# Kernel tuning notes

Hardware: AMD Instinct MI355X
Metric: run time of the kernel (lower is better)

## Reference

```python
import jax, jax.numpy as jnp
import numpy as np

NUM_HEADS = 16
HEAD_DIM = 64
EMBED_DIM = 1024
BSZ = 4
SEQ = 2048


def setup_inputs() -> dict:
    key = jax.random.key(0)
    ks = jax.random.split(key, 6)
    scale = 1.0 / np.sqrt(EMBED_DIM)
    return {
        "x": jax.random.normal(ks[0], (BSZ, SEQ, EMBED_DIM), jnp.float32),
        "rel_pos_bias": jax.random.normal(ks[1], (1, NUM_HEADS, SEQ, SEQ), jnp.float32),
        "Wq": jax.random.normal(ks[2], (EMBED_DIM, EMBED_DIM), jnp.float32) * scale,
        "Wk": jax.random.normal(ks[3], (EMBED_DIM, EMBED_DIM), jnp.float32) * scale,
        "Wv": jax.random.normal(ks[4], (EMBED_DIM, EMBED_DIM), jnp.float32) * scale,
        "Wo": jax.random.normal(ks[5], (EMBED_DIM, EMBED_DIM), jnp.float32) * scale,
    }


def reference(x, rel_pos_bias, Wq, Wk, Wv, Wo):
    b, s, e = x.shape
    h, d = NUM_HEADS, HEAD_DIM
    # projections (T5 linears have no bias); torch Linear: x @ W.T
    q = (x @ Wq.T).reshape(b, s, h, d).transpose(0, 2, 1, 3)  # [b,h,s,d]
    k = (x @ Wk.T).reshape(b, s, h, d).transpose(0, 2, 1, 3)
    v = (x @ Wv.T).reshape(b, s, h, d).transpose(0, 2, 1, 3)
    # unscaled attention scores + additive relative-position bias
    scores = jnp.einsum("bhqd,bhkd->bhqk", q, k) + rel_pos_bias  # [b,h,s,s]
    weights = jax.nn.softmax(scores.astype(jnp.float32), axis=-1).astype(scores.dtype)
    attn = jnp.einsum("bhqk,bhkd->bhqd", weights, v)  # [b,h,s,d]
    attn = attn.transpose(0, 2, 1, 3).reshape(b, s, e)
    return attn @ Wo.T
```

## Files before the change

kernel.cpp:

```cpp
#include <hip/hip_runtime.h>
#include <hip/hip_bf16.h>

#define NH 16
#define HD 64
#define ED 1024
#define BS 4
#define SL 2048

typedef _Float16 f16x8 __attribute__((ext_vector_type(8)));
typedef _Float16 f16x4 __attribute__((ext_vector_type(4)));
typedef _Float16 f16x2 __attribute__((ext_vector_type(2)));
typedef float floatx4 __attribute__((ext_vector_type(4)));

__global__ __launch_bounds__(256) void cvtw_kernel(const float* __restrict__ Wq,
                                                   const float* __restrict__ Wk,
                                                   const float* __restrict__ Wv,
                                                   _Float16* __restrict__ Wh)
{
    const float* W = (blockIdx.y == 0) ? Wq : (blockIdx.y == 1) ? Wk : Wv;
    _Float16* out = Wh + (size_t)blockIdx.y * (ED * ED);
    const int i = (blockIdx.x * 256 + threadIdx.x) * 4;
    float4 v = *(const float4*)(W + i);
    f16x4 c;
    c[0] = (_Float16)v.x; c[1] = (_Float16)v.y;
    c[2] = (_Float16)v.z; c[3] = (_Float16)v.w;
    *(f16x4*)(out + i) = c;
}

__device__ __forceinline__ int lds_boff(int kq, int rc)
{
    return (((kq << 7) + rc) << 4) ^ (kq << 5);
}

template <int A_MODE, int B_MODE, int OUT_MODE>
__device__ __forceinline__ void gemm128_body(const float* __restrict__ Af,
                                             const _Float16* __restrict__ Ah,
                                             const float* __restrict__ Bf,
                                             const _Float16* __restrict__ Bh,
                                             _Float16* __restrict__ outH,
                                             float* __restrict__ outF,
                                             int K, int N)
{
    __shared__ __align__(16) _Float16 As[4 * 128 * 8];
    __shared__ __align__(16) _Float16 Bs[4 * 128 * 8];

    const int tid  = threadIdx.x;
    const int wave = tid >> 6;
    const int lane = tid & 63;
    const int lo16 = lane & 15;
    const int hi4  = lane >> 4;
    const int wm = wave >> 1;
    const int wn = wave & 1;
    const int rowTile = blockIdx.y * 128;
    const int colTile = blockIdx.x * 128;

    floatx4 acc[4][4];
#pragma unroll
    for (int m = 0; m < 4; m++)
#pragma unroll
        for (int n = 0; n < 4; n++)
            acc[m][n] = (floatx4){0.f, 0.f, 0.f, 0.f};

    for (int kb = 0; kb < K; kb += 32) {
        float4 aF[4]; f16x8 aH[2];
        if (A_MODE == 0) {
#pragma unroll
            for (int r = 0; r < 4; r++) {
                const int t2 = tid + r * 256;
                const int row = t2 >> 3;
                const int k4 = (t2 & 7) * 4;
                aF[r] = *(const float4*)(Af + (size_t)(rowTile + row) * K + kb + k4);
            }
        } else {
#pragma unroll
            for (int r = 0; r < 2; r++) {
                const int t2 = tid + r * 256;
                const int row = t2 >> 2;
                const int ko = (t2 & 3) * 8;
                const int gr = rowTile + row;
                const int b = gr >> 11;
                const int s = gr & (SL - 1);
                const int k0 = kb + ko;
                const int h = k0 >> 6;
                const int d = k0 & (HD - 1);
                aH[r] = *(const f16x8*)(Ah + (((size_t)(b * NH + h)) * SL + s) * HD + d);
            }
        }
        f16x8 bH[2]; float4 bF[4];
        if (B_MODE == 0) {
#pragma unroll
            for (int r = 0; r < 2; r++) {
                const int t2 = tid + r * 256;
                const int col = t2 >> 2;
                const int ko = (t2 & 3) * 8;
                bH[r] = *(const f16x8*)(Bh + (size_t)(colTile + col) * K + kb + ko);
            }
        } else {
#pragma unroll
            for (int r = 0; r < 4; r++) {
                const int t2 = tid + r * 256;
                const int col = t2 >> 3;
                const int k4 = (t2 & 7) * 4;
                bF[r] = *(const float4*)(Bf + (size_t)(colTile + col) * K + kb + k4);
            }
        }

        __syncthreads();
        if (A_MODE == 0) {
#pragma unroll
            for (int r = 0; r < 4; r++) {
                const int t2 = tid + r * 256;
                const int row = t2 >> 3;
                const int k4 = (t2 & 7) * 4;
                f16x4 c;
                c[0] = (_Float16)aF[r].x; c[1] = (_Float16)aF[r].y;
                c[2] = (_Float16)aF[r].z; c[3] = (_Float16)aF[r].w;
                *(f16x4*)((char*)As + lds_boff(k4 >> 3, row) + (k4 & 7) * 2) = c;
            }
        } else {
#pragma unroll
            for (int r = 0; r < 2; r++) {
                const int t2 = tid + r * 256;
                const int row = t2 >> 2;
                const int ko = (t2 & 3) * 8;
                *(f16x8*)((char*)As + lds_boff(ko >> 3, row)) = aH[r];
            }
        }
        if (B_MODE == 0) {
#pragma unroll
            for (int r = 0; r < 2; r++) {
                const int t2 = tid + r * 256;
                const int col = t2 >> 2;
                const int ko = (t2 & 3) * 8;
                *(f16x8*)((char*)Bs + lds_boff(ko >> 3, col)) = bH[r];
            }
        } else {
#pragma unroll
            for (int r = 0; r < 4; r++) {
                const int t2 = tid + r * 256;
                const int col = t2 >> 3;
                const int k4 = (t2 & 7) * 4;
                f16x4 c;
                c[0] = (_Float16)bF[r].x; c[1] = (_Float16)bF[r].y;
                c[2] = (_Float16)bF[r].z; c[3] = (_Float16)bF[r].w;
                *(f16x4*)((char*)Bs + lds_boff(k4 >> 3, col) + (k4 & 7) * 2) = c;
            }
        }
        __syncthreads();

        f16x8 af[4], bfr[4];
#pragma unroll
        for (int m = 0; m < 4; m++)
            af[m] = *(const f16x8*)((char*)As + lds_boff(hi4, wm * 64 + m * 16 + lo16));
#pragma unroll
        for (int n = 0; n < 4; n++)
            bfr[n] = *(const f16x8*)((char*)Bs + lds_boff(hi4, wn * 64 + n * 16 + lo16));
#pragma unroll
        for (int m = 0; m < 4; m++)
#pragma unroll
            for (int n = 0; n < 4; n++)
                acc[m][n] = __builtin_amdgcn_mfma_f32_16x16x32_f16(af[m], bfr[n], acc[m][n], 0, 0, 0);
    }

#pragma unroll
    for (int m = 0; m < 4; m++) {
#pragma unroll
        for (int n = 0; n < 4; n++) {
            const int col = colTile + wn * 64 + n * 16 + lo16;
#pragma unroll
            for (int i = 0; i < 4; i++) {
                const int row = rowTile + wm * 64 + m * 16 + hi4 * 4 + i;
                float v = acc[m][n][i];
                if (OUT_MODE == 0) {
                    int b = row >> 11;
                    int s = row & (SL - 1);
                    int h = col >> 6;
                    int d = col & (HD - 1);
                    outH[(((size_t)(b * NH + h)) * SL + s) * HD + d] = (_Float16)v;
                } else {
                    outF[(size_t)row * N + col] = v;
                }
            }
        }
    }
}

__global__ __launch_bounds__(256) void qkv_kernel(const float* __restrict__ x,
                                                  const _Float16* __restrict__ Wh,
                                                  _Float16* __restrict__ Q,
                                                  _Float16* __restrict__ Kk,
                                                  _Float16* __restrict__ V)
{
    const _Float16* W = Wh + (size_t)blockIdx.z * (ED * ED);
    _Float16* out = (blockIdx.z == 0) ? Q : (blockIdx.z == 1) ? Kk : V;
    gemm128_body<0, 0, 0>(x, nullptr, nullptr, W, out, nullptr, ED, ED);
}

__global__ __launch_bounds__(256) void oproj_kernel(const _Float16* __restrict__ A,
                                                    const float* __restrict__ Wo,
                                                    float* __restrict__ out)
{
    gemm128_body<1, 1, 1>(nullptr, A, Wo, nullptr, nullptr, out, ED, ED);
}

__global__ __launch_bounds__(256) void attn_kernel(const _Float16* __restrict__ Qg,
                                                   const _Float16* __restrict__ Kg,
                                                   const _Float16* __restrict__ Vg,
                                                   const float* __restrict__ bias,
                                                   _Float16* __restrict__ attnOut)
{
    __shared__ __align__(16) _Float16 Ks[8 * 64 * 8];
    __shared__ __align__(16) _Float16 Vt[64 * 64];
    __shared__ __align__(16) _Float16 Ps[4 * 32 * 64];

    const int b  = blockIdx.x;
    const int qt = blockIdx.y;
    const int h  = blockIdx.z;
    const int bh = b * NH + h;
    const int tid  = threadIdx.x;
    const int wave = tid >> 6;
    const int lane = tid & 63;
    const int lo16 = lane & 15;
    const int hi4  = lane >> 4;

    const _Float16* Qbh = Qg + (size_t)bh * SL * HD;
    const _Float16* Kbh = Kg + (size_t)bh * SL * HD;
    const _Float16* Vbh = Vg + (size_t)bh * SL * HD;
    const float* biasH = bias + (size_t)h * SL * SL;

    const int q0 = qt * 128 + wave * 32;

    f16x8 qf[2][2];
#pragma unroll
    for (int m = 0; m < 2; m++)
#pragma unroll
        for (int ks = 0; ks < 2; ks++)
            qf[m][ks] = *(const f16x8*)(Qbh + (size_t)(q0 + m * 16 + lo16) * HD
                                        + ks * 32 + hi4 * 8);

    floatx4 oAcc[2][4];
    float mRow[2][4], lRow[2][4];
#pragma unroll
    for (int m = 0; m < 2; m++)
#pragma unroll
        for (int n = 0; n < 4; n++)
            oAcc[m][n] = (floatx4){0.f, 0.f, 0.f, 0.f};
#pragma unroll
    for (int m = 0; m < 2; m++)
#pragma unroll
        for (int r = 0; r < 4; r++) { mRow[m][r] = -1e30f; lRow[m][r] = 0.f; }

    const int kKey = tid >> 2;
    const int kD0  = (tid & 3) * 8;
    _Float16* kDst0 = Ks + (((kKey >> 4)     ) * 64 + (kKey & 15) + 16 * (kD0 >> 3)) * 8;
    _Float16* kDst1 = Ks + (((kKey >> 4) + 4) * 64 + (kKey & 15) + 16 * (kD0 >> 3)) * 8;

    const int vK0 = (tid >> 3) * 2;
    const int vD0 = (tid & 7) * 8;

    for (int kc = 0; kc < SL; kc += 64) {
        f16x8 ka = *(const f16x8*)(Kbh + (size_t)(kc + kKey) * HD + kD0);
        f16x8 kb = *(const f16x8*)(Kbh + (size_t)(kc + kKey) * HD + kD0 + 32);
        f16x8 va = *(const f16x8*)(Vbh + (size_t)(kc + vK0    ) * HD + vD0);
        f16x8 vb = *(const f16x8*)(Vbh + (size_t)(kc + vK0 + 1) * HD + vD0);

        __syncthreads();
        *(f16x8*)kDst0 = ka;
        *(f16x8*)kDst1 = kb;
#pragma unroll
        for (int i = 0; i < 8; i++) {
            const int d = vD0 + i;
            const int sw = (d & 7) ^ ((d >> 3) & 7);
            char* p = (char*)Vt + (d << 7)
                      + ((((vK0 >> 3) ^ sw) & 7) << 4) + ((vK0 & 7) << 1);
            f16x2 pr; pr[0] = va[i]; pr[1] = vb[i];
            *(f16x2*)p = pr;
        }
        __syncthreads();

        floatx4 s[2][4];
#pragma unroll
        for (int m = 0; m < 2; m++)
#pragma unroll
            for (int n = 0; n < 4; n++)
                s[m][n] = (floatx4){0.f, 0.f, 0.f, 0.f};
#pragma unroll
        for (int ks = 0; ks < 2; ks++)
#pragma unroll
            for (int n = 0; n < 4; n++) {
                f16x8 kf = *(const f16x8*)(Ks + ((ks * 4 + n) * 64 + lane) * 8);
                s[0][n] = __builtin_amdgcn_mfma_f32_16x16x32_f16(qf[0][ks], kf, s[0][n], 0, 0, 0);
                s[1][n] = __builtin_amdgcn_mfma_f32_16x16x32_f16(qf[1][ks], kf, s[1][n], 0, 0, 0);
            }

#pragma unroll
        for (int m = 0; m < 2; m++)
#pragma unroll
            for (int r = 0; r < 4; r++) {
                const int ql = m * 16 + hi4 * 4 + r;
                const float* bp = biasH + (size_t)(q0 + ql) * SL + kc + lo16;
                float s0 = s[m][0][r] + bp[0];
                float s1 = s[m][1][r] + bp[16];
                float s2 = s[m][2][r] + bp[32];
                float s3 = s[m][3][r] + bp[48];
                float rmax = fmaxf(fmaxf(s0, s1), fmaxf(s2, s3));
                rmax = fmaxf(rmax, __shfl_xor(rmax, 1));
                rmax = fmaxf(rmax, __shfl_xor(rmax, 2));
                rmax = fmaxf(rmax, __shfl_xor(rmax, 4));
                rmax = fmaxf(rmax, __shfl_xor(rmax, 8));
                const float mOld = mRow[m][r];
                const float mNew = fmaxf(mOld, rmax);
                const float alpha = __expf(mOld - mNew);
                mRow[m][r] = mNew;
                float p0 = __expf(s0 - mNew);
                float p1 = __expf(s1 - mNew);
                float p2 = __expf(s2 - mNew);
                float p3 = __expf(s3 - mNew);
                float rsum = (p0 + p1) + (p2 + p3);
                rsum += __shfl_xor(rsum, 1);
                rsum += __shfl_xor(rsum, 2);
                rsum += __shfl_xor(rsum, 4);
                rsum += __shfl_xor(rsum, 8);
                lRow[m][r] = lRow[m][r] * alpha + rsum;
#pragma unroll
                for (int n = 0; n < 4; n++) oAcc[m][n][r] *= alpha;

                char* pb = (char*)Ps + (wave << 12) + (ql << 7) + ((lo16 & 7) << 1);
                const int kb3 = lo16 >> 3;
                const int swp = (ql & 7) ^ (((ql >> 3) & 3) << 1);
                *(_Float16*)(pb + ((((0 + kb3) ^ swp) & 7) << 4)) = (_Float16)p0;
                *(_Float16*)(pb + ((((2 + kb3) ^ swp) & 7) << 4)) = (_Float16)p1;
                *(_Float16*)(pb + ((((4 + kb3) ^ swp) & 7) << 4)) = (_Float16)p2;
                *(_Float16*)(pb + ((((6 + kb3) ^ swp) & 7) << 4)) = (_Float16)p3;
            }

#pragma unroll
        for (int ks = 0; ks < 2; ks++) {
            f16x8 pa[2];
#pragma unroll
            for (int m = 0; m < 2; m++) {
                const int qlr = m * 16 + lo16;
                const int swp = (qlr & 7) ^ (((qlr >> 3) & 3) << 1);
                pa[m] = *(const f16x8*)((char*)Ps + (wave << 12) + (qlr << 7)
                                        + ((((ks * 4 + hi4) ^ swp) & 7) << 4));
            }
#pragma unroll
            for (int n = 0; n < 4; n++) {
                const int dv = n * 16 + lo16;
                const int swv = (dv & 7) ^ ((dv >> 3) & 7);
                f16x8 vf = *(const f16x8*)((char*)Vt + (dv << 7)
                                           + ((((ks * 4 + hi4) ^ swv) & 7) << 4));
                oAcc[0][n] = __builtin_amdgcn_mfma_f32_16x16x32_f16(pa[0], vf, oAcc[0][n], 0, 0, 0);
                oAcc[1][n] = __builtin_amdgcn_mfma_f32_16x16x32_f16(pa[1], vf, oAcc[1][n], 0, 0, 0);
            }
        }
    }

#pragma unroll
    for (int m = 0; m < 2; m++)
#pragma unroll
        for (int r = 0; r < 4; r++) {
            const float inv = 1.f / lRow[m][r];
            const int q = q0 + m * 16 + hi4 * 4 + r;
#pragma unroll
            for (int n = 0; n < 4; n++)
                attnOut[((size_t)bh * SL + q) * HD + n * 16 + lo16] =
                    (_Float16)(oAcc[m][n][r] * inv);
        }
}

extern "C" void kernel_launch(void* const* d_in, const int* in_sizes, int n_in,
                              void* d_out, int out_size, void* d_ws, size_t ws_size,
                              hipStream_t stream)
{
    (void)in_sizes; (void)n_in; (void)out_size; (void)ws_size;

    const float* x    = (const float*)d_in[0];
    const float* bias = (const float*)d_in[1];
    const float* Wq   = (const float*)d_in[2];
    const float* Wk   = (const float*)d_in[3];
    const float* Wv   = (const float*)d_in[4];
    const float* Wo   = (const float*)d_in[5];

    const size_t nQKV = (size_t)BS * NH * SL * HD;
    _Float16* Qh = (_Float16*)d_out;
    _Float16* Kh = Qh + nQKV;
    _Float16* Vh = (_Float16*)d_ws;
    _Float16* slotB = Vh + nQKV;
    _Float16* Wh = slotB;
    _Float16* attnH = slotB;

    cvtw_kernel<<<dim3(ED * ED / 1024, 3), 256, 0, stream>>>(Wq, Wk, Wv, Wh);

    dim3 gq(ED / 128, (BS * SL) / 128, 3);
    qkv_kernel<<<gq, 256, 0, stream>>>(x, Wh, Qh, Kh, Vh);

    dim3 ga(BS, SL / 128, NH);
    attn_kernel<<<ga, 256, 0, stream>>>(Qh, Kh, Vh, bias, attnH);

    dim3 go(ED / 128, (BS * SL) / 128);
    oproj_kernel<<<go, 256, 0, stream>>>(attnH, Wo, (float*)d_out);
}
```

Before: 747.6 us.

## Stage bias through LDS as fp16, prefetch K/V, lazy softmax rescale

The attention kernel now loads each 128x64 bias tile cooperatively with coalesced float4 reads, converts it to fp16 and stores it in a padded shared buffer instead of doing scattered per-lane global bias reads. K/V tiles for the next chunk are register-prefetched after the barrier so their loads overlap with compute. The online softmax skips the rescale unless the running max grows by more than 8, MFMA sections get raised wave priority, and the grid order is changed so q-tiles vary fastest. Rounding the bias to fp16 and deferring the rescale add numerical error, and the extra shared buffer may reduce occupancy.

```diff
diff --git a/kernel.cpp b/kernel.cpp
--- a/kernel.cpp
+++ b/kernel.cpp
@@ -212,9 +212,10 @@
     __shared__ __align__(16) _Float16 Ks[8 * 64 * 8];
     __shared__ __align__(16) _Float16 Vt[64 * 64];
     __shared__ __align__(16) _Float16 Ps[4 * 32 * 64];
-
-    const int b  = blockIdx.x;
-    const int qt = blockIdx.y;
+    __shared__ __align__(16) _Float16 Bi[128 * 68];
+
+    const int qt = blockIdx.x;
+    const int b  = blockIdx.y;
     const int h  = blockIdx.z;
     const int bh = b * NH + h;
     const int tid  = threadIdx.x;
@@ -254,15 +255,23 @@
     const int kD0  = (tid & 3) * 8;
     _Float16* kDst0 = Ks + (((kKey >> 4)     ) * 64 + (kKey & 15) + 16 * (kD0 >> 3)) * 8;
     _Float16* kDst1 = Ks + (((kKey >> 4) + 4) * 64 + (kKey & 15) + 16 * (kD0 >> 3)) * 8;
-
     const int vK0 = (tid >> 3) * 2;
     const int vD0 = (tid & 7) * 8;
 
+    const int bRow = tid >> 4;
+    const int bCol = (tid & 15) * 4;
+    const float* bThr = biasH + ((size_t)(qt * 128) + bRow) * SL + bCol;
+
+    f16x8 ka = *(const f16x8*)(Kbh + (size_t)(0 + kKey) * HD + kD0);
+    f16x8 kb = *(const f16x8*)(Kbh + (size_t)(0 + kKey) * HD + kD0 + 32);
+    f16x8 va = *(const f16x8*)(Vbh + (size_t)(0 + vK0    ) * HD + vD0);
+    f16x8 vb = *(const f16x8*)(Vbh + (size_t)(0 + vK0 + 1) * HD + vD0);
+
     for (int kc = 0; kc < SL; kc += 64) {
-        f16x8 ka = *(const f16x8*)(Kbh + (size_t)(kc + kKey) * HD + kD0);
-        f16x8 kb = *(const f16x8*)(Kbh + (size_t)(kc + kKey) * HD + kD0 + 32);
-        f16x8 va = *(const f16x8*)(Vbh + (size_t)(kc + vK0    ) * HD + vD0);
-        f16x8 vb = *(const f16x8*)(Vbh + (size_t)(kc + vK0 + 1) * HD + vD0);
+        float4 bld[8];
+#pragma unroll
+        for (int r = 0; r < 8; r++)
+            bld[r] = *(const float4*)(bThr + (size_t)r * 16 * SL + kc);
 
         __syncthreads();
         *(f16x8*)kDst0 = ka;
@@ -276,7 +285,22 @@
             f16x2 pr; pr[0] = va[i]; pr[1] = vb[i];
             *(f16x2*)p = pr;
         }
+#pragma unroll
+        for (int r = 0; r < 8; r++) {
+            f16x4 c;
+            c[0] = (_Float16)bld[r].x; c[1] = (_Float16)bld[r].y;
+            c[2] = (_Float16)bld[r].z; c[3] = (_Float16)bld[r].w;
+            *(f16x4*)(Bi + (bRow + r * 16) * 68 + bCol) = c;
+        }
         __syncthreads();
+
+        {
+            const int kn = (kc + 64 < SL) ? kc + 64 : kc;
+            ka = *(const f16x8*)(Kbh + (size_t)(kn + kKey) * HD + kD0);
+            kb = *(const f16x8*)(Kbh + (size_t)(kn + kKey) * HD + kD0 + 32);
+            va = *(const f16x8*)(Vbh + (size_t)(kn + vK0    ) * HD + vD0);
+            vb = *(const f16x8*)(Vbh + (size_t)(kn + vK0 + 1) * HD + vD0);
+        }
 
         floatx4 s[2][4];
 #pragma unroll
@@ -284,6 +308,7 @@
 #pragma unroll
             for (int n = 0; n < 4; n++)
                 s[m][n] = (floatx4){0.f, 0.f, 0.f, 0.f};
+        __builtin_amdgcn_s_setprio(1);
 #pragma unroll
         for (int ks = 0; ks < 2; ks++)
 #pragma unroll
@@ -292,38 +317,42 @@
                 s[0][n] = __builtin_amdgcn_mfma_f32_16x16x32_f16(qf[0][ks], kf, s[0][n], 0, 0, 0);
                 s[1][n] = __builtin_amdgcn_mfma_f32_16x16x32_f16(qf[1][ks], kf, s[1][n], 0, 0, 0);
             }
+        __builtin_amdgcn_s_setprio(0);
 
 #pragma unroll
         for (int m = 0; m < 2; m++)
 #pragma unroll
             for (int r = 0; r < 4; r++) {
                 const int ql = m * 16 + hi4 * 4 + r;
-                const float* bp = biasH + (size_t)(q0 + ql) * SL + kc + lo16;
-                float s0 = s[m][0][r] + bp[0];
-                float s1 = s[m][1][r] + bp[16];
-                float s2 = s[m][2][r] + bp[32];
-                float s3 = s[m][3][r] + bp[48];
+                const _Float16* bsr = Bi + (wave * 32 + ql) * 68;
+                float s0 = s[m][0][r] + (float)bsr[lo16];
+                float s1 = s[m][1][r] + (float)bsr[16 + lo16];
+                float s2 = s[m][2][r] + (float)bsr[32 + lo16];
+                float s3 = s[m][3][r] + (float)bsr[48 + lo16];
                 float rmax = fmaxf(fmaxf(s0, s1), fmaxf(s2, s3));
                 rmax = fmaxf(rmax, __shfl_xor(rmax, 1));
                 rmax = fmaxf(rmax, __shfl_xor(rmax, 2));
                 rmax = fmaxf(rmax, __shfl_xor(rmax, 4));
                 rmax = fmaxf(rmax, __shfl_xor(rmax, 8));
-                const float mOld = mRow[m][r];
-                const float mNew = fmaxf(mOld, rmax);
-                const float alpha = __expf(mOld - mNew);
-                mRow[m][r] = mNew;
-                float p0 = __expf(s0 - mNew);
-                float p1 = __expf(s1 - mNew);
-                float p2 = __expf(s2 - mNew);
-                float p3 = __expf(s3 - mNew);
+                float mCur = mRow[m][r];
+                if (rmax > mCur + 8.f) {
+                    const float alpha = __expf(mCur - rmax);
+                    mCur = rmax;
+                    mRow[m][r] = rmax;
+                    lRow[m][r] *= alpha;
+#pragma unroll
+                    for (int n = 0; n < 4; n++) oAcc[m][n][r] *= alpha;
+                }
+                float p0 = __expf(s0 - mCur);
+                float p1 = __expf(s1 - mCur);
+                float p2 = __expf(s2 - mCur);
+                float p3 = __expf(s3 - mCur);
                 float rsum = (p0 + p1) + (p2 + p3);
                 rsum += __shfl_xor(rsum, 1);
                 rsum += __shfl_xor(rsum, 2);
                 rsum += __shfl_xor(rsum, 4);
                 rsum += __shfl_xor(rsum, 8);
-                lRow[m][r] = lRow[m][r] * alpha + rsum;
-#pragma unroll
-                for (int n = 0; n < 4; n++) oAcc[m][n][r] *= alpha;
+                lRow[m][r] += rsum;
 
                 char* pb = (char*)Ps + (wave << 12) + (ql << 7) + ((lo16 & 7) << 1);
                 const int kb3 = lo16 >> 3;
@@ -334,6 +363,7 @@
                 *(_Float16*)(pb + ((((6 + kb3) ^ swp) & 7) << 4)) = (_Float16)p3;
             }
 
+        __builtin_amdgcn_s_setprio(1);
 #pragma unroll
         for (int ks = 0; ks < 2; ks++) {
             f16x8 pa[2];
@@ -354,6 +384,7 @@
                 oAcc[1][n] = __builtin_amdgcn_mfma_f32_16x16x32_f16(pa[1], vf, oAcc[1][n], 0, 0, 0);
             }
         }
+        __builtin_amdgcn_s_setprio(0);
     }
 
 #pragma unroll
@@ -395,7 +426,7 @@
     dim3 gq(ED / 128, (BS * SL) / 128, 3);
     qkv_kernel<<<gq, 256, 0, stream>>>(x, Wh, Qh, Kh, Vh);
 
-    dim3 ga(BS, SL / 128, NH);
+    dim3 ga(SL / 128, BS, NH);
     attn_kernel<<<ga, 256, 0, stream>>>(Qh, Kh, Vh, bias, attnH);
 
     dim3 go(ED / 128, (BS * SL) / 128);
```

After: 753.5 us. No clear change (+0.8%).
